# Optimization experiments

Hardware: AMD Instinct MI355X
Metric: run time of the kernel (lower is better)

## Reference

```python
import jax, jax.numpy as jnp
import numpy as np

B, HQ, HKV, QL, SL = 2, 32, 8, 1024, 4096
HEAD_DIM, HALF, ROPE, RANK = 128, 64, 64, 512


def setup_inputs() -> dict:
    key = jax.random.key(0)
    ks = jax.random.split(key, 6)
    return {
        "Q": jax.random.normal(ks[0], (B, HQ, QL, HEAD_DIM), jnp.float32),
        "C_kv_t2": jax.random.normal(ks[1], (B, SL, RANK), jnp.float32),
        "K_rope_t2": jax.random.normal(ks[2], (B, HKV, SL, ROPE), jnp.float32),
        "U_l": jax.random.normal(ks[3], (HALF, HALF), jnp.float32) / 8.0,
        "W_UK": jax.random.normal(ks[4], (HEAD_DIM - ROPE, RANK), jnp.float32) / 8.0,
        "W_UV": jax.random.normal(ks[5], (RANK, HEAD_DIM), jnp.float32) / 8.0,
    }


def reference(Q, C_kv_t2, K_rope_t2, U_l, W_UK, W_UV):
    # --- absorb_and_score ---
    # Rotate each half of Q by U_l (applied as x @ U_l.T)
    Qx, Qy = Q[..., :HALF], Q[..., HALF:]
    Q_rot = jnp.concatenate([Qx @ U_l.T, Qy @ U_l.T], axis=-1)  # [B,HQ,QL,HEAD_DIM]
    Q_rope = Q_rot[..., :ROPE]                                   # [B,HQ,QL,ROPE]
    Q_nope = Q_rot[..., ROPE:]                                   # [B,HQ,QL,nope_dim]
    Q_abs = Q_nope @ W_UK                                        # [B,HQ,QL,RANK]
    scores_nope = jnp.einsum('bhqr,bsr->bhqs', Q_abs, C_kv_t2)   # [B,HQ,QL,SL]
    # GQA: group q-heads per kv-head instead of materializing repeat_interleave
    g = HQ // HKV
    Qr_g = Q_rope.reshape(B, HKV, g, QL, ROPE)
    scores_rope = jnp.einsum('bkgqr,bksr->bkgqs', Qr_g, K_rope_t2)
    scores = scores_nope + scores_rope.reshape(B, HQ, QL, SL)
    # --- softmax glue + decompress_value ---
    weights = jax.nn.softmax(scores, axis=-1)                    # [B,HQ,QL,SL]
    out_latent = jnp.einsum('bhqs,bsr->bhqr', weights, C_kv_t2)  # [B,HQ,QL,RANK]
    out = out_latent @ W_UV                                      # [B,HQ,QL,HEAD_DIM]
    return out
```

## Files before the change

### kernel.cpp

```cpp
#include <hip/hip_runtime.h>
#include <stdint.h>

#define B_N   2
#define HQ_N  32
#define HKV_N 8
#define QL_N  1024
#define SL_N  4096
#define DH_N  128
#define ROPE_N 64
#define RANK_N 512

typedef _Float16 f16;
typedef _Float16 half8 __attribute__((ext_vector_type(8)));
typedef float floatx16 __attribute__((ext_vector_type(16)));
typedef int int2v __attribute__((ext_vector_type(2)));

union H8 { half8 h; uint64_t q[2]; };
union PKU { f16 h[2]; uint32_t u; };
union BFU { uint32_t u[4]; half8 h; };

__device__ inline half8 cvt8(float4 a, float4 b) {
  half8 o;
  o[0] = (f16)a.x; o[1] = (f16)a.y; o[2] = (f16)a.z; o[3] = (f16)a.w;
  o[4] = (f16)b.x; o[5] = (f16)b.y; o[6] = (f16)b.z; o[7] = (f16)b.w;
  return o;
}

__global__ __launch_bounds__(256) void k_convert(const float* __restrict__ Kr,
                                                 f16* __restrict__ Krf) {
  size_t idx = ((size_t)blockIdx.x * 256 + threadIdx.x) * 8;
  float4 a = *(const float4*)(Kr + idx);
  float4 b = *(const float4*)(Kr + idx + 4);
  *(half8*)(Krf + idx) = cvt8(a, b);
}

__global__ __launch_bounds__(256) void k_weights(const float* __restrict__ Ul,
                                                 const float* __restrict__ WUK,
                                                 const float* __restrict__ WUV,
                                                 f16* __restrict__ M2T2,
                                                 f16* __restrict__ WUKh,
                                                 f16* __restrict__ WUVT) {
  int idx = blockIdx.x * 256 + threadIdx.x;
  if (idx < 16384) {
    int c = idx >> 7, d = idx & 127;
    float v = 0.f;
    if (c < 64) { if (d >= 64) v = Ul[c * 64 + (d - 64)]; }
    else        { if (d < 64)  v = Ul[(c - 64) * 64 + d]; }
    M2T2[idx] = (f16)v;
  } else if (idx < 49152) {
    int i = idx - 16384;
    WUKh[i] = (f16)WUK[i];
  } else {
    int i = idx - 49152;
    int c = i >> 9, r = i & 511;
    WUVT[i] = (f16)WUV[r * 128 + c];
  }
}

__global__ __launch_bounds__(256) void k_qeff(const float* __restrict__ Q,
                                              const f16* __restrict__ M2T2,
                                              f16* __restrict__ Qeff2) {
  int t = threadIdx.x;
  int wave = t >> 6, lane = t & 63, l31 = lane & 31, lhi = lane >> 5;
  size_t q0 = (size_t)blockIdx.x * 128 + wave * 32;
  const float* qp = Q + (q0 + l31) * DH_N + lhi * 8;
  floatx16 acc[4];
#pragma unroll
  for (int ct = 0; ct < 4; ct++)
#pragma unroll
    for (int r = 0; r < 16; r++) acc[ct][r] = 0.f;
#pragma unroll
  for (int kk = 0; kk < 8; ++kk) {
    float4 a = *(const float4*)(qp + kk * 16);
    float4 b = *(const float4*)(qp + kk * 16 + 4);
    half8 af = cvt8(a, b);
#pragma unroll
    for (int ct = 0; ct < 4; ct++) {
      half8 bf = *(const half8*)(M2T2 + (size_t)(ct * 32 + l31) * 128 + kk * 16 + lhi * 8);
      acc[ct] = __builtin_amdgcn_mfma_f32_32x32x16_f16(af, bf, acc[ct], 0, 0, 0);
    }
  }
  const float LOG2E = 1.44269504f;
#pragma unroll
  for (int ct = 0; ct < 4; ct++)
#pragma unroll
    for (int r = 0; r < 16; r++) {
      int row = (r & 3) + 8 * (r >> 2) + 4 * lhi;
      Qeff2[(q0 + row) * 128 + ct * 32 + l31] = (f16)(acc[ct][r] * LOG2E);
    }
}

__global__ __launch_bounds__(256) void k_kncw(const float* __restrict__ C,
                                              const f16* __restrict__ WUKh,
                                              const f16* __restrict__ WUVT,
                                              f16* __restrict__ Kn,
                                              f16* __restrict__ CWT) {
  int t = threadIdx.x;
  int wave = t >> 6, lane = t & 63, l31 = lane & 31, lhi = lane >> 5;
  int b = blockIdx.x >> 5, st = blockIdx.x & 31;
  int s0 = st * 128 + wave * 32;
  const float* cp = C + ((size_t)b * SL_N + s0 + l31) * RANK_N + lhi * 8;
  floatx16 akn[2], acw[4];
#pragma unroll
  for (int ct = 0; ct < 2; ct++)
#pragma unroll
    for (int r = 0; r < 16; r++) akn[ct][r] = 0.f;
#pragma unroll
  for (int ct = 0; ct < 4; ct++)
#pragma unroll
    for (int r = 0; r < 16; r++) acw[ct][r] = 0.f;
#pragma unroll 4
  for (int kk = 0; kk < 32; ++kk) {
    float4 a = *(const float4*)(cp + kk * 16);
    float4 bq = *(const float4*)(cp + kk * 16 + 4);
    half8 cf = cvt8(a, bq);
#pragma unroll
    for (int ct = 0; ct < 2; ct++) {
      half8 bf = *(const half8*)(WUKh + (size_t)(ct * 32 + l31) * RANK_N + kk * 16 + lhi * 8);
      akn[ct] = __builtin_amdgcn_mfma_f32_32x32x16_f16(cf, bf, akn[ct], 0, 0, 0);
    }
#pragma unroll
    for (int ct = 0; ct < 4; ct++) {
      half8 af = *(const half8*)(WUVT + (size_t)(ct * 32 + l31) * RANK_N + kk * 16 + lhi * 8);
      acw[ct] = __builtin_amdgcn_mfma_f32_32x32x16_f16(af, cf, acw[ct], 0, 0, 0);
    }
  }
#pragma unroll
  for (int ct = 0; ct < 2; ct++)
#pragma unroll
    for (int r = 0; r < 16; r++) {
      int row = (r & 3) + 8 * (r >> 2) + 4 * lhi;
      Kn[((size_t)b * SL_N + s0 + row) * 64 + ct * 32 + l31] = (f16)akn[ct][r];
    }
#pragma unroll
  for (int ct = 0; ct < 4; ct++)
#pragma unroll
    for (int r = 0; r < 16; r++) {
      int row = (r & 3) + 8 * (r >> 2) + 4 * lhi;
      CWT[((size_t)b * DH_N + ct * 32 + row) * SL_N + s0 + l31] = (f16)acw[ct][r];
    }
}

#define KROW 132
#define CROW 68

__global__ __launch_bounds__(256, 2) void k_flash(
    const f16* __restrict__ Qeff2, const f16* __restrict__ Kn,
    const f16* __restrict__ Krf, const f16* __restrict__ CWT,
    float* __restrict__ out) {
  __shared__ __align__(16) char smem[51712];
  f16* kbuf  = (f16*)smem;
  f16* cbuf0 = (f16*)(smem + 16896);
  f16* cbuf1 = (f16*)(smem + 34304);
  float* ot  = (float*)smem;

  int t = threadIdx.x;
  int wave = t >> 6, lane = t & 63, l31 = lane & 31, lhi = lane >> 5;
  int qt = blockIdx.x & 7; int h = (blockIdx.x >> 3) & 31; int b = blockIdx.x >> 8;
  int kv = h >> 2;
  int qloc = wave * 32 + l31;

  const f16* Knb = Kn + (size_t)b * SL_N * 64;
  const f16* Kb  = Krf + (size_t)(b * HKV_N + kv) * SL_N * ROPE_N;
  const f16* Wb  = CWT + (size_t)b * DH_N * SL_N;

  half8 qf[8];
  {
    const f16* qrow = Qeff2 + ((size_t)(b * HQ_N + h) * QL_N + qt * 128 + qloc) * 128 + lhi * 8;
#pragma unroll
    for (int kk = 0; kk < 8; kk++) qf[kk] = *(const half8*)(qrow + kk * 16);
  }

  floatx16 oacc[4];
#pragma unroll
  for (int ct = 0; ct < 4; ct++)
#pragma unroll
    for (int r = 0; r < 16; r++) oacc[ct][r] = 0.f;
  float m_run = -1e30f, l_run = 0.f;

  int kr = t >> 3, kc = t & 7;
  int cA = t >> 2, cch = t & 3;
  const f16* pKn = Knb + (size_t)kr * 64 + kc * 8;
  const f16* pKr = Kb + (size_t)kr * ROPE_N + kc * 8;
  const f16* pW0 = Wb + (size_t)cA * SL_N;
  const f16* pW1 = Wb + (size_t)(64 + cA) * SL_N;
  int sw0 = ((cch) ^ (cA & 7)) * 8;
  int sw1 = ((cch + 4) ^ (cA & 7)) * 8;
  int rsw = l31 & 7;

  {
    H8 a0, a1, r0, r1, c0, c1, c2, c3;
    a0.h = *(const half8*)(pKn);
    a1.h = *(const half8*)(pKn + 32 * 64);
    r0.h = *(const half8*)(pKr);
    r1.h = *(const half8*)(pKr + 32 * ROPE_N);
    c0.h = *(const half8*)(pW0 + cch * 8);
    c1.h = *(const half8*)(pW0 + (cch + 4) * 8);
    c2.h = *(const half8*)(pW1 + cch * 8);
    c3.h = *(const half8*)(pW1 + (cch + 4) * 8);
    uint64_t* d;
    d = (uint64_t*)(kbuf + kr * KROW + kc * 8);              d[0] = a0.q[0]; d[1] = a0.q[1];
    d = (uint64_t*)(kbuf + (kr + 32) * KROW + kc * 8);       d[0] = a1.q[0]; d[1] = a1.q[1];
    d = (uint64_t*)(kbuf + kr * KROW + 64 + kc * 8);         d[0] = r0.q[0]; d[1] = r0.q[1];
    d = (uint64_t*)(kbuf + (kr + 32) * KROW + 64 + kc * 8);  d[0] = r1.q[0]; d[1] = r1.q[1];
    d = (uint64_t*)(cbuf0 + cA * CROW + sw0);                d[0] = c0.q[0]; d[1] = c0.q[1];
    d = (uint64_t*)(cbuf0 + cA * CROW + sw1);                d[0] = c1.q[0]; d[1] = c1.q[1];
    d = (uint64_t*)(cbuf0 + (64 + cA) * CROW + sw0);         d[0] = c2.q[0]; d[1] = c2.q[1];
    d = (uint64_t*)(cbuf0 + (64 + cA) * CROW + sw1);         d[0] = c3.q[0]; d[1] = c3.q[1];
  }
  __syncthreads();

  for (int it = 0; it < 64; ++it) {
    f16* cc = (it & 1) ? cbuf1 : cbuf0;
    f16* cn = (it & 1) ? cbuf0 : cbuf1;
    bool pre = it < 63;
    int s0n = (it + 1) * 64;
    H8 a0, a1, r0, r1, c0, c1, c2, c3;
    if (pre) {
      size_t ko = (size_t)s0n * 64;
      a0.h = *(const half8*)(pKn + ko);
      a1.h = *(const half8*)(pKn + ko + 32 * 64);
      r0.h = *(const half8*)(pKr + ko);
      r1.h = *(const half8*)(pKr + ko + 32 * ROPE_N);
      c0.h = *(const half8*)(pW0 + s0n + cch * 8);
      c1.h = *(const half8*)(pW0 + s0n + (cch + 4) * 8);
      c2.h = *(const half8*)(pW1 + s0n + cch * 8);
      c3.h = *(const half8*)(pW1 + s0n + (cch + 4) * 8);
    }

    floatx16 sa0, sa1;
#pragma unroll
    for (int r = 0; r < 16; r++) { sa0[r] = 0.f; sa1[r] = 0.f; }
    const f16* ka0 = kbuf + l31 * KROW + lhi * 8;
    const f16* ka1 = kbuf + (32 + l31) * KROW + lhi * 8;
#pragma unroll
    for (int kk = 0; kk < 8; kk++) {
      H8 x0, x1;
      const uint64_t* p0 = (const uint64_t*)(ka0 + kk * 16);
      const uint64_t* p1 = (const uint64_t*)(ka1 + kk * 16);
      x0.q[0] = p0[0]; x0.q[1] = p0[1];
      x1.q[0] = p1[0]; x1.q[1] = p1[1];
      sa0 = __builtin_amdgcn_mfma_f32_32x32x16_f16(x0.h, qf[kk], sa0, 0, 0, 0);
      sa1 = __builtin_amdgcn_mfma_f32_32x32x16_f16(x1.h, qf[kk], sa1, 0, 0, 0);
    }
    __syncthreads();

    if (pre) {
      uint64_t* d;
      d = (uint64_t*)(kbuf + kr * KROW + kc * 8);              d[0] = a0.q[0]; d[1] = a0.q[1];
      d = (uint64_t*)(kbuf + (kr + 32) * KROW + kc * 8);       d[0] = a1.q[0]; d[1] = a1.q[1];
      d = (uint64_t*)(kbuf + kr * KROW + 64 + kc * 8);         d[0] = r0.q[0]; d[1] = r0.q[1];
      d = (uint64_t*)(kbuf + (kr + 32) * KROW + 64 + kc * 8);  d[0] = r1.q[0]; d[1] = r1.q[1];
      d = (uint64_t*)(cn + cA * CROW + sw0);                   d[0] = c0.q[0]; d[1] = c0.q[1];
      d = (uint64_t*)(cn + cA * CROW + sw1);                   d[0] = c1.q[0]; d[1] = c1.q[1];
      d = (uint64_t*)(cn + (64 + cA) * CROW + sw0);            d[0] = c2.q[0]; d[1] = c2.q[1];
      d = (uint64_t*)(cn + (64 + cA) * CROW + sw1);            d[0] = c3.q[0]; d[1] = c3.q[1];
    }

    float mt = -1e30f;
#pragma unroll
    for (int r = 0; r < 16; r++) { mt = fmaxf(mt, sa0[r]); mt = fmaxf(mt, sa1[r]); }
    mt = fmaxf(mt, __shfl_xor(mt, 32, 64));
    if (__any(mt > m_run)) {
      float m_new = fmaxf(m_run, mt);
      float alpha = exp2f(m_run - m_new);
      l_run *= alpha;
#pragma unroll
      for (int ct = 0; ct < 4; ct++)
#pragma unroll
        for (int r = 0; r < 16; r++) oacc[ct][r] *= alpha;
      m_run = m_new;
    }
    float psum = 0.f;
#pragma unroll
    for (int r = 0; r < 16; r++) { sa0[r] = exp2f(sa0[r] - m_run); psum += sa0[r]; }
#pragma unroll
    for (int r = 0; r < 16; r++) { sa1[r] = exp2f(sa1[r] - m_run); psum += sa1[r]; }
    psum += __shfl_xor(psum, 32, 64);
    l_run += psum;

    half8 bfr0, bfr1, bfr2, bfr3;
    {
      uint32_t pk[8];
#pragma unroll
      for (int g = 0; g < 8; ++g) {
        PKU pu; pu.h[0] = (f16)sa0[2 * g]; pu.h[1] = (f16)sa0[2 * g + 1];
        pk[g] = pu.u;
      }
      int2v r0v = __builtin_amdgcn_permlane32_swap((int)pk[0], (int)pk[2], false, false);
      pk[0] = (uint32_t)r0v.x; pk[2] = (uint32_t)r0v.y;
      int2v r1v = __builtin_amdgcn_permlane32_swap((int)pk[1], (int)pk[3], false, false);
      pk[1] = (uint32_t)r1v.x; pk[3] = (uint32_t)r1v.y;
      int2v r2v = __builtin_amdgcn_permlane32_swap((int)pk[4], (int)pk[6], false, false);
      pk[4] = (uint32_t)r2v.x; pk[6] = (uint32_t)r2v.y;
      int2v r3v = __builtin_amdgcn_permlane32_swap((int)pk[5], (int)pk[7], false, false);
      pk[5] = (uint32_t)r3v.x; pk[7] = (uint32_t)r3v.y;
      BFU f0, f1;
      f0.u[0] = pk[0]; f0.u[1] = pk[1]; f0.u[2] = pk[2]; f0.u[3] = pk[3];
      f1.u[0] = pk[4]; f1.u[1] = pk[5]; f1.u[2] = pk[6]; f1.u[3] = pk[7];
      bfr0 = f0.h; bfr1 = f1.h;
    }
    {
      uint32_t pk[8];
#pragma unroll
      for (int g = 0; g < 8; ++g) {
        PKU pu; pu.h[0] = (f16)sa1[2 * g]; pu.h[1] = (f16)sa1[2 * g + 1];
        pk[g] = pu.u;
      }
      int2v r0v = __builtin_amdgcn_permlane32_swap((int)pk[0], (int)pk[2], false, false);
      pk[0] = (uint32_t)r0v.x; pk[2] = (uint32_t)r0v.y;
      int2v r1v = __builtin_amdgcn_permlane32_swap((int)pk[1], (int)pk[3], false, false);
      pk[1] = (uint32_t)r1v.x; pk[3] = (uint32_t)r1v.y;
      int2v r2v = __builtin_amdgcn_permlane32_swap((int)pk[4], (int)pk[6], false, false);
      pk[4] = (uint32_t)r2v.x; pk[6] = (uint32_t)r2v.y;
      int2v r3v = __builtin_amdgcn_permlane32_swap((int)pk[5], (int)pk[7], false, false);
      pk[5] = (uint32_t)r3v.x; pk[7] = (uint32_t)r3v.y;
      BFU f0, f1;
      f0.u[0] = pk[0]; f0.u[1] = pk[1]; f0.u[2] = pk[2]; f0.u[3] = pk[3];
      f1.u[0] = pk[4]; f1.u[1] = pk[5]; f1.u[2] = pk[6]; f1.u[3] = pk[7];
      bfr2 = f0.h; bfr3 = f1.h;
    }

#pragma unroll
    for (int ks = 0; ks < 4; ++ks) {
      half8 bfh = (ks == 0) ? bfr0 : (ks == 1) ? bfr1 : (ks == 2) ? bfr2 : bfr3;
#pragma unroll
      for (int ct = 0; ct < 4; ct++) {
        H8 af;
        const uint64_t* pa = (const uint64_t*)(cc + (ct * 32 + l31) * CROW +
                                               (((ks * 2 + lhi) ^ rsw) * 8));
        af.q[0] = pa[0]; af.q[1] = pa[1];
        oacc[ct] = __builtin_amdgcn_mfma_f32_32x32x16_f16(af.h, bfh, oacc[ct], 0, 0, 0);
      }
    }
    __syncthreads();
  }

  float inv = 1.0f / l_run;
  float* outp = out + ((size_t)(b * HQ_N + h) * QL_N + qt * 128) * DH_N;
#pragma unroll
  for (int p = 0; p < 2; ++p) {
    __syncthreads();
    if ((qloc >> 6) == p) {
      int lr = qloc & 63;
#pragma unroll
      for (int ct = 0; ct < 4; ct++)
#pragma unroll
        for (int r = 0; r < 16; r++) {
          int c = ct * 32 + (r & 3) + 8 * (r >> 2) + 4 * lhi;
          ot[lr * 133 + c] = oacc[ct][r] * inv;
        }
    }
    __syncthreads();
#pragma unroll
    for (int i = 0; i < 8; i++) {
      int flat = i * 256 + t; int q = flat >> 5, ch = flat & 31;
      float4 v;
      v.x = ot[q * 133 + ch * 4 + 0];
      v.y = ot[q * 133 + ch * 4 + 1];
      v.z = ot[q * 133 + ch * 4 + 2];
      v.w = ot[q * 133 + ch * 4 + 3];
      *(float4*)(outp + (size_t)(p * 64 + q) * DH_N + ch * 4) = v;
    }
  }
}

extern "C" void kernel_launch(void* const* d_in, const int* in_sizes, int n_in,
                              void* d_out, int out_size, void* d_ws, size_t ws_size,
                              hipStream_t stream) {
  (void)in_sizes; (void)n_in; (void)out_size; (void)ws_size;
  const float* Q   = (const float*)d_in[0];
  const float* C   = (const float*)d_in[1];
  const float* Kr  = (const float*)d_in[2];
  const float* Ul  = (const float*)d_in[3];
  const float* WUK = (const float*)d_in[4];
  const float* WUV = (const float*)d_in[5];
  float* out = (float*)d_out;
  char* ws = (char*)d_ws;
  f16* Qeff2 = (f16*)ws;
  f16* Krf   = (f16*)(ws + 16777216);
  f16* CWT   = (f16*)(ws + 25165824);
  f16* Kn    = (f16*)(ws + 27262976);
  f16* M2T2  = (f16*)(ws + 28311552);
  f16* WUKh  = (f16*)(ws + 28344320);
  f16* WUVT  = (f16*)(ws + 28409856);

  hipLaunchKernelGGL(k_convert, dim3(2048), dim3(256), 0, stream, Kr, Krf);
  hipLaunchKernelGGL(k_weights, dim3(448),  dim3(256), 0, stream, Ul, WUK, WUV, M2T2, WUKh, WUVT);
  hipLaunchKernelGGL(k_qeff,    dim3(512),  dim3(256), 0, stream, Q, M2T2, Qeff2);
  hipLaunchKernelGGL(k_kncw,    dim3(64),   dim3(256), 0, stream, C, WUKh, WUVT, Kn, CWT);
  hipLaunchKernelGGL(k_flash,   dim3(512),  dim3(256), 0, stream, Qeff2, Kn, Krf, CWT, out);
}
```

Before: 338.5 us.

## Fuse Q projection into flash kernel, split kncw work across waves, reorder softmax

Removes the separate k_qeff kernel and computes the rotated, log2e-scaled Q tile inside k_flash, staging it through shared memory, which avoids a 16MB fp16 round trip and one launch. k_kncw now runs 256 blocks, with each wave handling one 32-row sequence tile and a subset of output columns, so more blocks fill the GPU. In the flash loop, the softmax and PV MFMAs now run before the next tile's shared-memory stores, wrapped in s_setprio hints. exp2f is replaced with the hardware exp2 builtin and f16 packing uses cvt_pkrtz. The added prologue work and extra syncs in k_flash could lengthen each block.

After: 287.7 us. 15.0% less time.

```diff
diff --git a/kernel.cpp b/kernel.cpp
--- a/kernel.cpp
+++ b/kernel.cpp
@@ -12,11 +12,12 @@
 
 typedef _Float16 f16;
 typedef _Float16 half8 __attribute__((ext_vector_type(8)));
+typedef __fp16 fp16x2 __attribute__((ext_vector_type(2)));
 typedef float floatx16 __attribute__((ext_vector_type(16)));
 typedef int int2v __attribute__((ext_vector_type(2)));
 
 union H8 { half8 h; uint64_t q[2]; };
-union PKU { f16 h[2]; uint32_t u; };
+union PK2 { fp16x2 h; uint32_t u; };
 union BFU { uint32_t u[4]; half8 h; };
 
 __device__ inline half8 cvt8(float4 a, float4 b) {
@@ -57,39 +58,6 @@
   }
 }
 
-__global__ __launch_bounds__(256) void k_qeff(const float* __restrict__ Q,
-                                              const f16* __restrict__ M2T2,
-                                              f16* __restrict__ Qeff2) {
-  int t = threadIdx.x;
-  int wave = t >> 6, lane = t & 63, l31 = lane & 31, lhi = lane >> 5;
-  size_t q0 = (size_t)blockIdx.x * 128 + wave * 32;
-  const float* qp = Q + (q0 + l31) * DH_N + lhi * 8;
-  floatx16 acc[4];
-#pragma unroll
-  for (int ct = 0; ct < 4; ct++)
-#pragma unroll
-    for (int r = 0; r < 16; r++) acc[ct][r] = 0.f;
-#pragma unroll
-  for (int kk = 0; kk < 8; ++kk) {
-    float4 a = *(const float4*)(qp + kk * 16);
-    float4 b = *(const float4*)(qp + kk * 16 + 4);
-    half8 af = cvt8(a, b);
-#pragma unroll
-    for (int ct = 0; ct < 4; ct++) {
-      half8 bf = *(const half8*)(M2T2 + (size_t)(ct * 32 + l31) * 128 + kk * 16 + lhi * 8);
-      acc[ct] = __builtin_amdgcn_mfma_f32_32x32x16_f16(af, bf, acc[ct], 0, 0, 0);
-    }
-  }
-  const float LOG2E = 1.44269504f;
-#pragma unroll
-  for (int ct = 0; ct < 4; ct++)
-#pragma unroll
-    for (int r = 0; r < 16; r++) {
-      int row = (r & 3) + 8 * (r >> 2) + 4 * lhi;
-      Qeff2[(q0 + row) * 128 + ct * 32 + l31] = (f16)(acc[ct][r] * LOG2E);
-    }
-}
-
 __global__ __launch_bounds__(256) void k_kncw(const float* __restrict__ C,
                                               const f16* __restrict__ WUKh,
                                               const f16* __restrict__ WUVT,
@@ -97,61 +65,76 @@
                                               f16* __restrict__ CWT) {
   int t = threadIdx.x;
   int wave = t >> 6, lane = t & 63, l31 = lane & 31, lhi = lane >> 5;
-  int b = blockIdx.x >> 5, st = blockIdx.x & 31;
-  int s0 = st * 128 + wave * 32;
+  int b = blockIdx.x >> 7, st = blockIdx.x & 127;
+  int s0 = st * 32;
   const float* cp = C + ((size_t)b * SL_N + s0 + l31) * RANK_N + lhi * 8;
-  floatx16 akn[2], acw[4];
-#pragma unroll
-  for (int ct = 0; ct < 2; ct++)
-#pragma unroll
-    for (int r = 0; r < 16; r++) akn[ct][r] = 0.f;
-#pragma unroll
-  for (int ct = 0; ct < 4; ct++)
-#pragma unroll
-    for (int r = 0; r < 16; r++) acw[ct][r] = 0.f;
+  floatx16 a0, a1;
+#pragma unroll
+  for (int r = 0; r < 16; r++) { a0[r] = 0.f; a1[r] = 0.f; }
 #pragma unroll 4
   for (int kk = 0; kk < 32; ++kk) {
-    float4 a = *(const float4*)(cp + kk * 16);
-    float4 bq = *(const float4*)(cp + kk * 16 + 4);
-    half8 cf = cvt8(a, bq);
-#pragma unroll
-    for (int ct = 0; ct < 2; ct++) {
-      half8 bf = *(const half8*)(WUKh + (size_t)(ct * 32 + l31) * RANK_N + kk * 16 + lhi * 8);
-      akn[ct] = __builtin_amdgcn_mfma_f32_32x32x16_f16(cf, bf, akn[ct], 0, 0, 0);
-    }
-#pragma unroll
-    for (int ct = 0; ct < 4; ct++) {
-      half8 af = *(const half8*)(WUVT + (size_t)(ct * 32 + l31) * RANK_N + kk * 16 + lhi * 8);
-      acw[ct] = __builtin_amdgcn_mfma_f32_32x32x16_f16(af, cf, acw[ct], 0, 0, 0);
-    }
-  }
-#pragma unroll
-  for (int ct = 0; ct < 2; ct++)
+    float4 fa = *(const float4*)(cp + kk * 16);
+    float4 fb = *(const float4*)(cp + kk * 16 + 4);
+    half8 cf = cvt8(fa, fb);
+    if (wave == 0) {
+      half8 b0 = *(const half8*)(WUKh + (size_t)l31 * RANK_N + kk * 16 + lhi * 8);
+      half8 b1 = *(const half8*)(WUKh + (size_t)(32 + l31) * RANK_N + kk * 16 + lhi * 8);
+      a0 = __builtin_amdgcn_mfma_f32_32x32x16_f16(cf, b0, a0, 0, 0, 0);
+      a1 = __builtin_amdgcn_mfma_f32_32x32x16_f16(cf, b1, a1, 0, 0, 0);
+    } else if (wave == 1) {
+      half8 w0 = *(const half8*)(WUVT + (size_t)l31 * RANK_N + kk * 16 + lhi * 8);
+      a0 = __builtin_amdgcn_mfma_f32_32x32x16_f16(w0, cf, a0, 0, 0, 0);
+    } else if (wave == 2) {
+      half8 w1 = *(const half8*)(WUVT + (size_t)(32 + l31) * RANK_N + kk * 16 + lhi * 8);
+      half8 w2 = *(const half8*)(WUVT + (size_t)(64 + l31) * RANK_N + kk * 16 + lhi * 8);
+      a0 = __builtin_amdgcn_mfma_f32_32x32x16_f16(w1, cf, a0, 0, 0, 0);
+      a1 = __builtin_amdgcn_mfma_f32_32x32x16_f16(w2, cf, a1, 0, 0, 0);
+    } else {
+      half8 w3 = *(const half8*)(WUVT + (size_t)(96 + l31) * RANK_N + kk * 16 + lhi * 8);
+      a0 = __builtin_amdgcn_mfma_f32_32x32x16_f16(w3, cf, a0, 0, 0, 0);
+    }
+  }
+  if (wave == 0) {
 #pragma unroll
     for (int r = 0; r < 16; r++) {
       int row = (r & 3) + 8 * (r >> 2) + 4 * lhi;
-      Kn[((size_t)b * SL_N + s0 + row) * 64 + ct * 32 + l31] = (f16)akn[ct][r];
-    }
-#pragma unroll
-  for (int ct = 0; ct < 4; ct++)
+      Kn[((size_t)b * SL_N + s0 + row) * 64 + l31]      = (f16)a0[r];
+      Kn[((size_t)b * SL_N + s0 + row) * 64 + 32 + l31] = (f16)a1[r];
+    }
+  } else if (wave == 1) {
 #pragma unroll
     for (int r = 0; r < 16; r++) {
       int row = (r & 3) + 8 * (r >> 2) + 4 * lhi;
-      CWT[((size_t)b * DH_N + ct * 32 + row) * SL_N + s0 + l31] = (f16)acw[ct][r];
-    }
+      CWT[((size_t)b * DH_N + row) * SL_N + s0 + l31] = (f16)a0[r];
+    }
+  } else if (wave == 2) {
+#pragma unroll
+    for (int r = 0; r < 16; r++) {
+      int row = (r & 3) + 8 * (r >> 2) + 4 * lhi;
+      CWT[((size_t)b * DH_N + 32 + row) * SL_N + s0 + l31] = (f16)a0[r];
+      CWT[((size_t)b * DH_N + 64 + row) * SL_N + s0 + l31] = (f16)a1[r];
+    }
+  } else {
+#pragma unroll
+    for (int r = 0; r < 16; r++) {
+      int row = (r & 3) + 8 * (r >> 2) + 4 * lhi;
+      CWT[((size_t)b * DH_N + 96 + row) * SL_N + s0 + l31] = (f16)a0[r];
+    }
+  }
 }
 
 #define KROW 132
 #define CROW 68
 
 __global__ __launch_bounds__(256, 2) void k_flash(
-    const f16* __restrict__ Qeff2, const f16* __restrict__ Kn,
-    const f16* __restrict__ Krf, const f16* __restrict__ CWT,
-    float* __restrict__ out) {
+    const float* __restrict__ Q, const f16* __restrict__ M2T2,
+    const f16* __restrict__ Kn, const f16* __restrict__ Krf,
+    const f16* __restrict__ CWT, float* __restrict__ out) {
   __shared__ __align__(16) char smem[51712];
   f16* kbuf  = (f16*)smem;
   f16* cbuf0 = (f16*)(smem + 16896);
   f16* cbuf1 = (f16*)(smem + 34304);
+  f16* qs    = (f16*)smem;
   float* ot  = (float*)smem;
 
   int t = threadIdx.x;
@@ -163,20 +146,6 @@
   const f16* Knb = Kn + (size_t)b * SL_N * 64;
   const f16* Kb  = Krf + (size_t)(b * HKV_N + kv) * SL_N * ROPE_N;
   const f16* Wb  = CWT + (size_t)b * DH_N * SL_N;
-
-  half8 qf[8];
-  {
-    const f16* qrow = Qeff2 + ((size_t)(b * HQ_N + h) * QL_N + qt * 128 + qloc) * 128 + lhi * 8;
-#pragma unroll
-    for (int kk = 0; kk < 8; kk++) qf[kk] = *(const half8*)(qrow + kk * 16);
-  }
-
-  floatx16 oacc[4];
-#pragma unroll
-  for (int ct = 0; ct < 4; ct++)
-#pragma unroll
-    for (int r = 0; r < 16; r++) oacc[ct][r] = 0.f;
-  float m_run = -1e30f, l_run = 0.f;
 
   int kr = t >> 3, kc = t & 7;
   int cA = t >> 2, cch = t & 3;
@@ -188,16 +157,51 @@
   int sw1 = ((cch + 4) ^ (cA & 7)) * 8;
   int rsw = l31 & 7;
 
+  H8 a0, a1, r0, r1, c0, c1, c2, c3;
+  a0.h = *(const half8*)(pKn);
+  a1.h = *(const half8*)(pKn + 32 * 64);
+  r0.h = *(const half8*)(pKr);
+  r1.h = *(const half8*)(pKr + 32 * ROPE_N);
+  c0.h = *(const half8*)(pW0 + cch * 8);
+  c1.h = *(const half8*)(pW0 + (cch + 4) * 8);
+  c2.h = *(const half8*)(pW1 + cch * 8);
+  c3.h = *(const half8*)(pW1 + (cch + 4) * 8);
+
   {
-    H8 a0, a1, r0, r1, c0, c1, c2, c3;
-    a0.h = *(const half8*)(pKn);
-    a1.h = *(const half8*)(pKn + 32 * 64);
-    r0.h = *(const half8*)(pKr);
-    r1.h = *(const half8*)(pKr + 32 * ROPE_N);
-    c0.h = *(const half8*)(pW0 + cch * 8);
-    c1.h = *(const half8*)(pW0 + (cch + 4) * 8);
-    c2.h = *(const half8*)(pW1 + cch * 8);
-    c3.h = *(const half8*)(pW1 + (cch + 4) * 8);
+    const float* qp = Q + ((size_t)(b * HQ_N + h) * QL_N + qt * 128 + wave * 32 + l31) * DH_N + lhi * 8;
+    floatx16 acc[4];
+#pragma unroll
+    for (int ct = 0; ct < 4; ct++)
+#pragma unroll
+      for (int r = 0; r < 16; r++) acc[ct][r] = 0.f;
+#pragma unroll
+    for (int kk = 0; kk < 8; ++kk) {
+      float4 fa = *(const float4*)(qp + kk * 16);
+      float4 fb = *(const float4*)(qp + kk * 16 + 4);
+      half8 af = cvt8(fa, fb);
+#pragma unroll
+      for (int ct = 0; ct < 4; ct++) {
+        half8 bf = *(const half8*)(M2T2 + (size_t)(ct * 32 + l31) * 128 + kk * 16 + lhi * 8);
+        acc[ct] = __builtin_amdgcn_mfma_f32_32x32x16_f16(af, bf, acc[ct], 0, 0, 0);
+      }
+    }
+    const float LOG2E = 1.44269504f;
+#pragma unroll
+    for (int ct = 0; ct < 4; ct++)
+#pragma unroll
+      for (int r = 0; r < 16; r++) {
+        int row = (r & 3) + 8 * (r >> 2) + 4 * lhi;
+        qs[(wave * 32 + row) * 132 + ct * 32 + l31] = (f16)(acc[ct][r] * LOG2E);
+      }
+  }
+  __syncthreads();
+  half8 qf[8];
+#pragma unroll
+  for (int kk = 0; kk < 8; kk++)
+    qf[kk] = *(const half8*)(qs + (size_t)qloc * 132 + kk * 16 + lhi * 8);
+  __syncthreads();
+
+  {
     uint64_t* d;
     d = (uint64_t*)(kbuf + kr * KROW + kc * 8);              d[0] = a0.q[0]; d[1] = a0.q[1];
     d = (uint64_t*)(kbuf + (kr + 32) * KROW + kc * 8);       d[0] = a1.q[0]; d[1] = a1.q[1];
@@ -210,12 +214,18 @@
   }
   __syncthreads();
 
+  floatx16 oacc[4];
+#pragma unroll
+  for (int ct = 0; ct < 4; ct++)
+#pragma unroll
+    for (int r = 0; r < 16; r++) oacc[ct][r] = 0.f;
+  float m_run = -1e30f, l_run = 0.f;
+
   for (int it = 0; it < 64; ++it) {
     f16* cc = (it & 1) ? cbuf1 : cbuf0;
     f16* cn = (it & 1) ? cbuf0 : cbuf1;
     bool pre = it < 63;
     int s0n = (it + 1) * 64;
-    H8 a0, a1, r0, r1, c0, c1, c2, c3;
     if (pre) {
       size_t ko = (size_t)s0n * 64;
       a0.h = *(const half8*)(pKn + ko);
@@ -233,6 +243,7 @@
     for (int r = 0; r < 16; r++) { sa0[r] = 0.f; sa1[r] = 0.f; }
     const f16* ka0 = kbuf + l31 * KROW + lhi * 8;
     const f16* ka1 = kbuf + (32 + l31) * KROW + lhi * 8;
+    __builtin_amdgcn_s_setprio(1);
 #pragma unroll
     for (int kk = 0; kk < 8; kk++) {
       H8 x0, x1;
@@ -243,7 +254,87 @@
       sa0 = __builtin_amdgcn_mfma_f32_32x32x16_f16(x0.h, qf[kk], sa0, 0, 0, 0);
       sa1 = __builtin_amdgcn_mfma_f32_32x32x16_f16(x1.h, qf[kk], sa1, 0, 0, 0);
     }
+    __builtin_amdgcn_s_setprio(0);
     __syncthreads();
+
+    float mt = -1e30f;
+#pragma unroll
+    for (int r = 0; r < 16; r++) { mt = fmaxf(mt, sa0[r]); mt = fmaxf(mt, sa1[r]); }
+    mt = fmaxf(mt, __shfl_xor(mt, 32, 64));
+    if (__any(mt > m_run)) {
+      float m_new = fmaxf(m_run, mt);
+      float alpha = __builtin_amdgcn_exp2f(m_run - m_new);
+      l_run *= alpha;
+#pragma unroll
+      for (int ct = 0; ct < 4; ct++)
+#pragma unroll
+        for (int r = 0; r < 16; r++) oacc[ct][r] *= alpha;
+      m_run = m_new;
+    }
+    float psum = 0.f;
+#pragma unroll
+    for (int r = 0; r < 16; r++) { sa0[r] = __builtin_amdgcn_exp2f(sa0[r] - m_run); psum += sa0[r]; }
+#pragma unroll
+    for (int r = 0; r < 16; r++) { sa1[r] = __builtin_amdgcn_exp2f(sa1[r] - m_run); psum += sa1[r]; }
+    psum += __shfl_xor(psum, 32, 64);
+    l_run += psum;
+
+    half8 bfr0, bfr1, bfr2, bfr3;
+    {
+      uint32_t pk[8];
+#pragma unroll
+      for (int g = 0; g < 8; ++g) {
+        PK2 pu; pu.h = __builtin_amdgcn_cvt_pkrtz(sa0[2 * g], sa0[2 * g + 1]);
+        pk[g] = pu.u;
+      }
+      int2v v0 = __builtin_amdgcn_permlane32_swap((int)pk[0], (int)pk[2], false, false);
+      pk[0] = (uint32_t)v0.x; pk[2] = (uint32_t)v0.y;
+      int2v v1 = __builtin_amdgcn_permlane32_swap((int)pk[1], (int)pk[3], false, false);
+      pk[1] = (uint32_t)v1.x; pk[3] = (uint32_t)v1.y;
+      int2v v2 = __builtin_amdgcn_permlane32_swap((int)pk[4], (int)pk[6], false, false);
+      pk[4] = (uint32_t)v2.x; pk[6] = (uint32_t)v2.y;
+      int2v v3 = __builtin_amdgcn_permlane32_swap((int)pk[5], (int)pk[7], false, false);
+      pk[5] = (uint32_t)v3.x; pk[7] = (uint32_t)v3.y;
+      BFU f0, f1;
+      f0.u[0] = pk[0]; f0.u[1] = pk[1]; f0.u[2] = pk[2]; f0.u[3] = pk[3];
+      f1.u[0] = pk[4]; f1.u[1] = pk[5]; f1.u[2] = pk[6]; f1.u[3] = pk[7];
+      bfr0 = f0.h; bfr1 = f1.h;
+    }
+    {
+      uint32_t pk[8];
+#pragma unroll
+      for (int g = 0; g < 8; ++g) {
+        PK2 pu; pu.h = __builtin_amdgcn_cvt_pkrtz(sa1[2 * g], sa1[2 * g + 1]);
+        pk[g] = pu.u;
+      }
+      int2v v0 = __builtin_amdgcn_permlane32_swap((int)pk[0], (int)pk[2], false, false);
+      pk[0] = (uint32_t)v0.x; pk[2] = (uint32_t)v0.y;
+      int2v v1 = __builtin_amdgcn_permlane32_swap((int)pk[1], (int)pk[3], false, false);
+      pk[1] = (uint32_t)v1.x; pk[3] = (uint32_t)v1.y;
+      int2v v2 = __builtin_amdgcn_permlane32_swap((int)pk[4], (int)pk[6], false, false);
+      pk[4] = (uint32_t)v2.x; pk[6] = (uint32_t)v2.y;
+      int2v v3 = __builtin_amdgcn_permlane32_swap((int)pk[5], (int)pk[7], false, false);
+      pk[5] = (uint32_t)v3.x; pk[7] = (uint32_t)v3.y;
+      BFU f0, f1;
+      f0.u[0] = pk[0]; f0.u[1] = pk[1]; f0.u[2] = pk[2]; f0.u[3] = pk[3];
+      f1.u[0] = pk[4]; f1.u[1] = pk[5]; f1.u[2] = pk[6]; f1.u[3] = pk[7];
+      bfr2 = f0.h; bfr3 = f1.h;
+    }
+
+    __builtin_amdgcn_s_setprio(1);
+#pragma unroll
+    for (int ks = 0; ks < 4; ++ks) {
+      half8 bfh = (ks == 0) ? bfr0 : (ks == 1) ? bfr1 : (ks == 2) ? bfr2 : bfr3;
+#pragma unroll
+      for (int ct = 0; ct < 4; ct++) {
+        H8 af;
+        const uint64_t* pa = (const uint64_t*)(cc + (ct * 32 + l31) * CROW +
+                                               (((ks * 2 + lhi) ^ rsw) * 8));
+        af.q[0] = pa[0]; af.q[1] = pa[1];
+        oacc[ct] = __builtin_amdgcn_mfma_f32_32x32x16_f16(af.h, bfh, oacc[ct], 0, 0, 0);
+      }
+    }
+    __builtin_amdgcn_s_setprio(0);
 
     if (pre) {
       uint64_t* d;
@@ -255,83 +346,6 @@
       d = (uint64_t*)(cn + cA * CROW + sw1);                   d[0] = c1.q[0]; d[1] = c1.q[1];
       d = (uint64_t*)(cn + (64 + cA) * CROW + sw0);            d[0] = c2.q[0]; d[1] = c2.q[1];
       d = (uint64_t*)(cn + (64 + cA) * CROW + sw1);            d[0] = c3.q[0]; d[1] = c3.q[1];
-    }
-
-    float mt = -1e30f;
-#pragma unroll
-    for (int r = 0; r < 16; r++) { mt = fmaxf(mt, sa0[r]); mt = fmaxf(mt, sa1[r]); }
-    mt = fmaxf(mt, __shfl_xor(mt, 32, 64));
-    if (__any(mt > m_run)) {
-      float m_new = fmaxf(m_run, mt);
-      float alpha = exp2f(m_run - m_new);
-      l_run *= alpha;
-#pragma unroll
-      for (int ct = 0; ct < 4; ct++)
-#pragma unroll
-        for (int r = 0; r < 16; r++) oacc[ct][r] *= alpha;
-      m_run = m_new;
-    }
-    float psum = 0.f;
-#pragma unroll
-    for (int r = 0; r < 16; r++) { sa0[r] = exp2f(sa0[r] - m_run); psum += sa0[r]; }
-#pragma unroll
-    for (int r = 0; r < 16; r++) { sa1[r] = exp2f(sa1[r] - m_run); psum += sa1[r]; }
-    psum += __shfl_xor(psum, 32, 64);
-    l_run += psum;
-
-    half8 bfr0, bfr1, bfr2, bfr3;
-    {
-      uint32_t pk[8];
-#pragma unroll
-      for (int g = 0; g < 8; ++g) {
-        PKU pu; pu.h[0] = (f16)sa0[2 * g]; pu.h[1] = (f16)sa0[2 * g + 1];
-        pk[g] = pu.u;
-      }
-      int2v r0v = __builtin_amdgcn_permlane32_swap((int)pk[0], (int)pk[2], false, false);
-      pk[0] = (uint32_t)r0v.x; pk[2] = (uint32_t)r0v.y;
-      int2v r1v = __builtin_amdgcn_permlane32_swap((int)pk[1], (int)pk[3], false, false);
-      pk[1] = (uint32_t)r1v.x; pk[3] = (uint32_t)r1v.y;
-      int2v r2v = __builtin_amdgcn_permlane32_swap((int)pk[4], (int)pk[6], false, false);
-      pk[4] = (uint32_t)r2v.x; pk[6] = (uint32_t)r2v.y;
-      int2v r3v = __builtin_amdgcn_permlane32_swap((int)pk[5], (int)pk[7], false, false);
-      pk[5] = (uint32_t)r3v.x; pk[7] = (uint32_t)r3v.y;
-      BFU f0, f1;
-      f0.u[0] = pk[0]; f0.u[1] = pk[1]; f0.u[2] = pk[2]; f0.u[3] = pk[3];
-      f1.u[0] = pk[4]; f1.u[1] = pk[5]; f1.u[2] = pk[6]; f1.u[3] = pk[7];
-      bfr0 = f0.h; bfr1 = f1.h;
-    }
-    {
-      uint32_t pk[8];
-#pragma unroll
-      for (int g = 0; g < 8; ++g) {
-        PKU pu; pu.h[0] = (f16)sa1[2 * g]; pu.h[1] = (f16)sa1[2 * g + 1];
-        pk[g] = pu.u;
-      }
-      int2v r0v = __builtin_amdgcn_permlane32_swap((int)pk[0], (int)pk[2], false, false);
-      pk[0] = (uint32_t)r0v.x; pk[2] = (uint32_t)r0v.y;
-      int2v r1v = __builtin_amdgcn_permlane32_swap((int)pk[1], (int)pk[3], false, false);
-      pk[1] = (uint32_t)r1v.x; pk[3] = (uint32_t)r1v.y;
-      int2v r2v = __builtin_amdgcn_permlane32_swap((int)pk[4], (int)pk[6], false, false);
-      pk[4] = (uint32_t)r2v.x; pk[6] = (uint32_t)r2v.y;
-      int2v r3v = __builtin_amdgcn_permlane32_swap((int)pk[5], (int)pk[7], false, false);
-      pk[5] = (uint32_t)r3v.x; pk[7] = (uint32_t)r3v.y;
-      BFU f0, f1;
-      f0.u[0] = pk[0]; f0.u[1] = pk[1]; f0.u[2] = pk[2]; f0.u[3] = pk[3];
-      f1.u[0] = pk[4]; f1.u[1] = pk[5]; f1.u[2] = pk[6]; f1.u[3] = pk[7];
-      bfr2 = f0.h; bfr3 = f1.h;
-    }
-
-#pragma unroll
-    for (int ks = 0; ks < 4; ++ks) {
-      half8 bfh = (ks == 0) ? bfr0 : (ks == 1) ? bfr1 : (ks == 2) ? bfr2 : bfr3;
-#pragma unroll
-      for (int ct = 0; ct < 4; ct++) {
-        H8 af;
-        const uint64_t* pa = (const uint64_t*)(cc + (ct * 32 + l31) * CROW +
-                                               (((ks * 2 + lhi) ^ rsw) * 8));
-        af.q[0] = pa[0]; af.q[1] = pa[1];
-        oacc[ct] = __builtin_amdgcn_mfma_f32_32x32x16_f16(af.h, bfh, oacc[ct], 0, 0, 0);
-      }
     }
     __syncthreads();
   }
@@ -377,17 +391,15 @@
   const float* WUV = (const float*)d_in[5];
   float* out = (float*)d_out;
   char* ws = (char*)d_ws;
-  f16* Qeff2 = (f16*)ws;
-  f16* Krf   = (f16*)(ws + 16777216);
-  f16* CWT   = (f16*)(ws + 25165824);
-  f16* Kn    = (f16*)(ws + 27262976);
-  f16* M2T2  = (f16*)(ws + 28311552);
-  f16* WUKh  = (f16*)(ws + 28344320);
-  f16* WUVT  = (f16*)(ws + 28409856);
+  f16* Krf   = (f16*)ws;
+  f16* CWT   = (f16*)(ws + 8388608);
+  f16* Kn    = (f16*)(ws + 10485760);
+  f16* M2T2  = (f16*)(ws + 11534336);
+  f16* WUKh  = (f16*)(ws + 11567104);
+  f16* WUVT  = (f16*)(ws + 11632640);
 
   hipLaunchKernelGGL(k_convert, dim3(2048), dim3(256), 0, stream, Kr, Krf);
   hipLaunchKernelGGL(k_weights, dim3(448),  dim3(256), 0, stream, Ul, WUK, WUV, M2T2, WUKh, WUVT);
-  hipLaunchKernelGGL(k_qeff,    dim3(512),  dim3(256), 0, stream, Q, M2T2, Qeff2);
-  hipLaunchKernelGGL(k_kncw,    dim3(64),   dim3(256), 0, stream, C, WUKh, WUVT, Kn, CWT);
-  hipLaunchKernelGGL(k_flash,   dim3(512),  dim3(256), 0, stream, Qeff2, Kn, Krf, CWT, out);
-}
+  hipLaunchKernelGGL(k_kncw,    dim3(256),  dim3(256), 0, stream, C, WUKh, WUVT, Kn, CWT);
+  hipLaunchKernelGGL(k_flash,   dim3(512),  dim3(256), 0, stream, Q, M2T2, Kn, Krf, CWT, out);
+}
```
